# Kernel optimization log

Measured on AMD Instinct MI355X. Metric: run time of the kernel, lower is better.

## Reference

```python
import jax, jax.numpy as jnp
import numpy as np

D_MODEL = 1024
N_HEADS_Q = 16
N_HEADS_KV = 4
D_HEAD = 64  # d_qk = d_v
THETA = 10000.0
CLAMP = 80.0


def apply_rope(x, theta=THETA):
    # x: (b, h, s, d) with d even; interleaved-pair rotary embedding
    b, h, s, d = x.shape
    inv_freq = 1.0 / (theta ** (jnp.arange(0, d, 2, dtype=jnp.float32) / d))  # (d/2,)
    ang = jnp.arange(s, dtype=jnp.float32)[:, None] * inv_freq[None, :]       # (s, d/2)
    cos, sin = jnp.cos(ang), jnp.sin(ang)
    x1, x2 = x[..., 0::2], x[..., 1::2]
    o1 = x1 * cos - x2 * sin
    o2 = x1 * sin + x2 * cos
    return jnp.stack([o1, o2], axis=-1).reshape(b, h, s, d).astype(x.dtype)


def setup_inputs() -> dict:
    key = jax.random.key(0)
    k0, k1, k2, k3, k4 = jax.random.split(key, 5)
    scale = 1.0 / np.sqrt(D_MODEL)
    return {
        "x": jax.random.normal(k0, (2, 2048, D_MODEL), dtype=jnp.float32),
        "Wq": jax.random.normal(k1, (N_HEADS_Q * D_HEAD, D_MODEL), dtype=jnp.float32) * scale,
        "Wk": jax.random.normal(k2, (N_HEADS_KV * D_HEAD, D_MODEL), dtype=jnp.float32) * scale,
        "Wv": jax.random.normal(k3, (N_HEADS_KV * D_HEAD, D_MODEL), dtype=jnp.float32) * scale,
        "Wo": jax.random.normal(k4, (D_MODEL, N_HEADS_Q * D_HEAD), dtype=jnp.float32) * scale,
    }


def _attention(x, Wq, Wk, Wv, Wo):
    b, s, _ = x.shape
    r = N_HEADS_Q // N_HEADS_KV  # queries per KV group
    # projections (Linear: y = x @ W^T, no bias)
    Q = (x @ Wq.T).reshape(b, s, N_HEADS_Q, D_HEAD).transpose(0, 2, 1, 3)   # (b, Hq, s, d)
    K = (x @ Wk.T).reshape(b, s, N_HEADS_KV, D_HEAD).transpose(0, 2, 1, 3)  # (b, Hkv, s, d)
    V = (x @ Wv.T).reshape(b, s, N_HEADS_KV, D_HEAD).transpose(0, 2, 1, 3)
    Q = apply_rope(Q)
    K = apply_rope(K)
    # GQA grouping: (b, Hkv, r, s, d)
    Qg = Q.reshape(b, N_HEADS_KV, r, s, D_HEAD)
    scores = jnp.einsum('bgrqd,bgkd->bgrqk', Qg, K)          # (b, g, r, s, s)
    scores = jnp.clip(scores, -CLAMP, CLAMP)
    causal = jnp.tril(jnp.ones((s, s), dtype=bool))
    scores = jnp.where(causal, scores, -jnp.inf)
    weights = jax.nn.softmax(scores / jnp.sqrt(jnp.float32(D_HEAD)), axis=-1)
    attn = jnp.einsum('bgrqk,bgkd->bgrqd', weights, V)       # (b, g, r, s, d)
    # '... h_kv r s d -> ... s (h_kv r d)'
    attn = attn.transpose(0, 3, 1, 2, 4).reshape(b, s, N_HEADS_Q * D_HEAD)
    return attn @ Wo.T


def reference(x, Wq, Wk, Wv, Wo):
    return _attention(x, Wq, Wk, Wv, Wo)
```

## Files before the change

kernel.cpp:

```cpp
#include <hip/hip_runtime.h>
#include <hip/hip_bf16.h>
#include <math.h>

typedef __attribute__((ext_vector_type(8))) short bf16x8;
typedef __attribute__((ext_vector_type(4))) float f32x4;

#define B_   2
#define S_   2048
#define DM   1024
#define HQ   16
#define HKV  4
#define DH   64

#define MFMA16(a, b, c) __builtin_amdgcn_mfma_f32_16x16x32_bf16(a, b, c, 0, 0, 0)

__device__ __forceinline__ void load_lds16(const __hip_bfloat16* g, __hip_bfloat16* l)
{
    __builtin_amdgcn_global_load_lds(
        (const __attribute__((address_space(1))) unsigned int*)g,
        (__attribute__((address_space(3))) unsigned int*)l, 16, 0, 0);
}

#define CVT_TOTAL 6815744
__global__ void cvt_all(const float* __restrict__ x,  const float* __restrict__ wq,
                        const float* __restrict__ wk, const float* __restrict__ wv,
                        const float* __restrict__ wo,
                        __hip_bfloat16* __restrict__ xb,  __hip_bfloat16* __restrict__ wqb,
                        __hip_bfloat16* __restrict__ wkb, __hip_bfloat16* __restrict__ wvb,
                        __hip_bfloat16* __restrict__ wob)
{
    int i = (blockIdx.x * blockDim.x + threadIdx.x) * 4;
    if (i >= CVT_TOTAL) return;
    const float* src; __hip_bfloat16* dst; int off;
    if      (i < 4194304) { src = x;  dst = xb;  off = 0; }
    else if (i < 5242880) { src = wq; dst = wqb; off = 4194304; }
    else if (i < 5505024) { src = wk; dst = wkb; off = 5242880; }
    else if (i < 5767168) { src = wv; dst = wvb; off = 5505024; }
    else                  { src = wo; dst = wob; off = 5767168; }
    i -= off;
    float4 v = *(const float4*)(src + i);
    union { ushort4 u; __hip_bfloat16 h[4]; } p;
    p.h[0] = __float2bfloat16(v.x);
    p.h[1] = __float2bfloat16(v.y);
    p.h[2] = __float2bfloat16(v.z);
    p.h[3] = __float2bfloat16(v.w);
    *(ushort4*)(dst + i) = p.u;
}

template <bool QKV>
__global__ __launch_bounds__(256, 3) void gemm_tile(
    const __hip_bfloat16* __restrict__ A,
    const __hip_bfloat16* __restrict__ W,
    float* __restrict__ C0, __hip_bfloat16* __restrict__ Qb,
    __hip_bfloat16* __restrict__ Kb, __hip_bfloat16* __restrict__ Vt, int K)
{
    const int wave = threadIdx.x >> 6;
    const int lane = threadIdx.x & 63;
    const int quad = lane >> 4;
    const int l16  = lane & 15;
    const int wm = wave >> 1, wn = wave & 1;
    const int m0 = blockIdx.x * 64;
    const int n0 = blockIdx.y * 128;

    __shared__ __align__(16) __hip_bfloat16 As[64 * 32];
    __shared__ __align__(16) __hip_bfloat16 Bs[128 * 32];

    f32x4 acc[2][4] = {};

    for (int k0 = 0; k0 < K; k0 += 32) {
        #pragma unroll
        for (int r = 0; r < 3; ++r) {
            const int m = wave * 3 + r;
            if (m < 4) {
                const int g = m * 64 + lane;
                const int row = g >> 2;
                const int cbs = ((g & 3) - row) & 3;
                load_lds16(A + (size_t)(m0 + row) * K + k0 + cbs * 8, &As[m * 512]);
            } else {
                const int g = (m - 4) * 64 + lane;
                const int row = g >> 2;
                const int cbs = ((g & 3) - row) & 3;
                load_lds16(W + (size_t)(n0 + row) * K + k0 + cbs * 8, &Bs[(m - 4) * 512]);
            }
        }
        __syncthreads();
        bf16x8 af[2], bf[4];
        #pragma unroll
        for (int i = 0; i < 2; ++i) {
            const int ra = wm * 32 + i * 16 + l16;
            af[i] = *(const bf16x8*)&As[ra * 32 + ((quad + ra) & 3) * 8];
        }
        #pragma unroll
        for (int j = 0; j < 4; ++j) {
            const int rb = wn * 64 + j * 16 + l16;
            bf[j] = *(const bf16x8*)&Bs[rb * 32 + ((quad + rb) & 3) * 8];
        }
        #pragma unroll
        for (int i = 0; i < 2; ++i)
            #pragma unroll
            for (int j = 0; j < 4; ++j)
                acc[i][j] = MFMA16(af[i], bf[j], acc[i][j]);
        __syncthreads();
    }

    #pragma unroll
    for (int j = 0; j < 4; ++j) {
        const int cbase = n0 + wn * 64 + j * 16;
        const int cb = cbase + l16;
        if (QKV && cbase < 1280) {
            const int ii = (cb >> 1) & 31;
            const float f = exp2f((float)ii * -0.41524101186092f);
            const float f_rev = f * 0.15915494309189535f;
            const bool odd = cb & 1;
            #pragma unroll
            for (int i = 0; i < 2; ++i) {
                #pragma unroll
                for (int reg = 0; reg < 4; ++reg) {
                    const int row = m0 + wm * 32 + i * 16 + quad * 4 + reg;
                    const float v = acc[i][j][reg];
                    const float p = __shfl_xor(v, 1);
                    float rev = (float)(row & (S_ - 1)) * f_rev;
                    rev -= floorf(rev);
                    const float sn = __builtin_amdgcn_sinf(rev);
                    const float cs = __builtin_amdgcn_cosf(rev);
                    const float o = odd ? (p * sn + v * cs) : (v * cs - p * sn);
                    if (cbase < 1024)
                        Qb[(size_t)row * 1024 + cb] = __float2bfloat16(o);
                    else
                        Kb[(size_t)row * 256 + cb - 1024] = __float2bfloat16(o);
                }
            }
        } else {
            #pragma unroll
            for (int i = 0; i < 2; ++i) {
                #pragma unroll
                for (int reg = 0; reg < 4; ++reg) {
                    const int row = m0 + wm * 32 + i * 16 + quad * 4 + reg;
                    const float v = acc[i][j][reg];
                    if (QKV)
                        Vt[((size_t)(row >> 11) * 256 + (cb - 1280)) * S_ +
                           (row & (S_ - 1))] = __float2bfloat16(v);
                    else
                        C0[(size_t)row * 1024 + cb] = v;
                }
            }
        }
    }
}

template <bool MASKED>
__device__ __forceinline__ void softmax_store(
    const f32x4* sacc, int q, int k0, int quad, int l16,
    float& lsum, __hip_bfloat16* PsTile)
{
    #pragma unroll
    for (int nt = 0; nt < 4; ++nt) {
        union { ushort4 u; __hip_bfloat16 h[4]; } pk;
        #pragma unroll
        for (int reg = 0; reg < 4; ++reg) {
            const float sc = fminf(fmaxf(sacc[nt][reg], -80.0f), 80.0f);
            float p = exp2f(fmaf(sc, 0.18033688011112042f,
                                 -14.426950408889634f));
            if (MASKED) {
                const int key = k0 + nt * 16 + quad * 4 + reg;
                p = (key <= q) ? p : 0.0f;
            }
            lsum += p;
            pk.h[reg] = __float2bfloat16(p);
        }
        *(ushort4*)&PsTile[l16 * 72 + nt * 16 + quad * 4] = pk.u;
    }
}

__global__ __launch_bounds__(256, 2) void attn_mfma(
    const __hip_bfloat16* __restrict__ Q,
    const __hip_bfloat16* __restrict__ K,
    const __hip_bfloat16* __restrict__ Vt,
    __hip_bfloat16* __restrict__ ctx)
{
    const int t    = blockIdx.x & 15;
    const int hq   = (blockIdx.x >> 4) & (HQ - 1);
    const int b    = blockIdx.x >> 8;
    const int hkv  = hq >> 2;
    const int wave = threadIdx.x >> 6;
    const int lane = threadIdx.x & 63;
    const int quad = lane >> 4;
    const int l16  = lane & 15;

    const int qlo = t * 64 + wave * 16 + l16;
    const int qhi = (31 - t) * 64 + wave * 16 + l16;

    __shared__ __align__(16) __hip_bfloat16 Ks[2][64 * 64];
    __shared__ __align__(16) __hip_bfloat16 Vs[2][64 * 64];
    __shared__ __align__(16) __hip_bfloat16 Ps[4][2][16 * 72];

    const __hip_bfloat16* qpl = Q + ((size_t)(b * S_) + qlo) * (HQ * DH) + hq * DH + quad * 8;
    const __hip_bfloat16* qph = Q + ((size_t)(b * S_) + qhi) * (HQ * DH) + hq * DH + quad * 8;
    bf16x8 ql0 = *(const bf16x8*)qpl;
    bf16x8 ql1 = *(const bf16x8*)(qpl + 32);
    bf16x8 qh0 = *(const bf16x8*)qph;
    bf16x8 qh1 = *(const bf16x8*)(qph + 32);

    const __hip_bfloat16* Kg = K + (size_t)(b * S_) * (HKV * DH) + hkv * DH;
    const __hip_bfloat16* Vg = Vt + (size_t)(b * HKV + hkv) * DH * S_;

    auto stage = [&](int sb, int k0s) {
        #pragma unroll
        for (int r = 0; r < 2; ++r) {
            const int m = wave * 2 + r;
            const int g = m * 64 + lane;
            const int row = g >> 3;
            const int cbs = ((g & 7) - row) & 7;
            load_lds16(Kg + (size_t)(k0s + row) * (HKV * DH) + cbs * 8, &Ks[sb][m * 512]);
            load_lds16(Vg + (size_t)row * S_ + k0s + cbs * 8, &Vs[sb][m * 512]);
        }
    };

    stage(0, 0);

    float lsum_lo = 0.0f, lsum_hi = 0.0f;
    f32x4 Olo[4] = {}, Ohi[4] = {};
    const f32x4 zro = {0.0f, 0.0f, 0.0f, 0.0f};

    const int last = 31 - t;
    for (int kt = 0; kt <= last; ++kt) {
        const int buf = kt & 1;
        const int k0 = kt * 64;
        __syncthreads();
        if (kt < last) stage(buf ^ 1, k0 + 64);
        const bool dual = (kt <= t);

        bf16x8 ka[4][2];
        #pragma unroll
        for (int nt = 0; nt < 4; ++nt) {
            const int key = nt * 16 + l16;
            ka[nt][0] = *(const bf16x8*)&Ks[buf][key * 64 + ((quad + key) & 7) * 8];
            ka[nt][1] = *(const bf16x8*)&Ks[buf][key * 64 + ((quad + 4 + key) & 7) * 8];
        }
        f32x4 shi[4], slo[4];
        #pragma unroll
        for (int nt = 0; nt < 4; ++nt) {
            shi[nt] = MFMA16(ka[nt][0], qh0, zro);
            shi[nt] = MFMA16(ka[nt][1], qh1, shi[nt]);
        }
        if (dual) {
            #pragma unroll
            for (int nt = 0; nt < 4; ++nt) {
                slo[nt] = MFMA16(ka[nt][0], ql0, zro);
                slo[nt] = MFMA16(ka[nt][1], ql1, slo[nt]);
            }
        }

        if (kt == last) softmax_store<true >(shi, qhi, k0, quad, l16, lsum_hi, &Ps[wave][1][0]);
        else            softmax_store<false>(shi, qhi, k0, quad, l16, lsum_hi, &Ps[wave][1][0]);
        if (dual) {
            if (kt == t) softmax_store<true >(slo, qlo, k0, quad, l16, lsum_lo, &Ps[wave][0][0]);
            else         softmax_store<false>(slo, qlo, k0, quad, l16, lsum_lo, &Ps[wave][0][0]);
        }
        __asm__ __volatile__("s_waitcnt lgkmcnt(0)" ::: "memory");

        bf16x8 va[2][4];
        #pragma unroll
        for (int ks = 0; ks < 2; ++ks)
            #pragma unroll
            for (int dt = 0; dt < 4; ++dt) {
                const int d = dt * 16 + l16;
                va[ks][dt] = *(const bf16x8*)
                    &Vs[buf][d * 64 + ((ks * 4 + quad + d) & 7) * 8];
            }
        #pragma unroll
        for (int ks = 0; ks < 2; ++ks) {
            bf16x8 pb = *(const bf16x8*)&Ps[wave][1][l16 * 72 + ks * 32 + quad * 8];
            #pragma unroll
            for (int dt = 0; dt < 4; ++dt)
                Ohi[dt] = MFMA16(va[ks][dt], pb, Ohi[dt]);
        }
        if (dual) {
            #pragma unroll
            for (int ks = 0; ks < 2; ++ks) {
                bf16x8 pb = *(const bf16x8*)&Ps[wave][0][l16 * 72 + ks * 32 + quad * 8];
                #pragma unroll
                for (int dt = 0; dt < 4; ++dt)
                    Olo[dt] = MFMA16(va[ks][dt], pb, Olo[dt]);
            }
        }
    }

    auto finish = [&](float lsum, const f32x4* O, int qrow) {
        lsum += __shfl_xor(lsum, 16);
        lsum += __shfl_xor(lsum, 32);
        const float inv = 1.0f / lsum;
        __hip_bfloat16* cp =
            ctx + ((size_t)(b * S_) + qrow) * (HQ * DH) + hq * DH + quad * 4;
        #pragma unroll
        for (int dt = 0; dt < 4; ++dt) {
            union { ushort4 u; __hip_bfloat16 h[4]; } o;
            #pragma unroll
            for (int reg = 0; reg < 4; ++reg)
                o.h[reg] = __float2bfloat16(O[dt][reg] * inv);
            *(ushort4*)(cp + dt * 16) = o.u;
        }
    };
    finish(lsum_lo, Olo, qlo);
    finish(lsum_hi, Ohi, qhi);
}

extern "C" void kernel_launch(void* const* d_in, const int* in_sizes, int n_in,
                              void* d_out, int out_size, void* d_ws, size_t ws_size,
                              hipStream_t stream)
{
    const float* x  = (const float*)d_in[0];
    const float* Wq = (const float*)d_in[1];
    const float* Wk = (const float*)d_in[2];
    const float* Wv = (const float*)d_in[3];
    const float* Wo = (const float*)d_in[4];
    float* out = (float*)d_out;

    const int M = B_ * S_;

    char* w = (char*)d_ws;
    __hip_bfloat16* xb    = (__hip_bfloat16*)w;  w += (size_t)M * DM * 2;
    __hip_bfloat16* Wqkvb = (__hip_bfloat16*)w;  w += (size_t)1536 * DM * 2;
    __hip_bfloat16* Wob   = (__hip_bfloat16*)w;  w += (size_t)DM * (HQ * DH) * 2;
    __hip_bfloat16* Qb16  = (__hip_bfloat16*)w;  w += (size_t)M * (HQ * DH) * 2;
    __hip_bfloat16* Kb16  = (__hip_bfloat16*)w;  w += (size_t)M * (HKV * DH) * 2;
    __hip_bfloat16* Vt    = (__hip_bfloat16*)w;  w += (size_t)M * (HKV * DH) * 2;
    __hip_bfloat16* ctx   = (__hip_bfloat16*)w;

    __hip_bfloat16* Wqb = Wqkvb;
    __hip_bfloat16* Wkb = Wqkvb + (size_t)1024 * 1024;
    __hip_bfloat16* Wvb = Wqkvb + (size_t)1280 * 1024;

    cvt_all<<<(CVT_TOTAL / 4 + 255) / 256, 256, 0, stream>>>(
        x, Wq, Wk, Wv, Wo, xb, Wqb, Wkb, Wvb, Wob);

    gemm_tile<true><<<dim3(M / 64, 1536 / 128), 256, 0, stream>>>(
        xb, Wqkvb, nullptr, Qb16, Kb16, Vt, DM);

    attn_mfma<<<B_ * HQ * 16, 256, 0, stream>>>(Qb16, Kb16, Vt, ctx);

    gemm_tile<false><<<dim3(M / 64, 1024 / 128), 256, 0, stream>>>(
        ctx, Wob, out, nullptr, nullptr, nullptr, HQ * DH);
}
```

Baseline: 174.0 us.

## Enlarge GEMM tiles to 128x128x64 with double-buffered LDS staging

Rewrites the projection GEMM kernel to use 128x128 output tiles with a K-step of 64, so each wave computes a 4x4 grid of MFMA tiles. Global-to-LDS loads go into a double buffer, so the next K-slice is fetched while the current one is computed, and the barrier count per K-step drops. Per-tile data reuse improves, but block counts are halved (256 and 384 blocks) and LDS/register use rise, which lowers occupancy (launch bounds become 2).

```diff
diff --git a/kernel.cpp b/kernel.cpp
--- a/kernel.cpp
+++ b/kernel.cpp
@@ -48,7 +48,7 @@
 }
 
 template <bool QKV>
-__global__ __launch_bounds__(256, 3) void gemm_tile(
+__global__ __launch_bounds__(256, 2) void gemm_tile(
     const __hip_bfloat16* __restrict__ A,
     const __hip_bfloat16* __restrict__ W,
     float* __restrict__ C0, __hip_bfloat16* __restrict__ Qb,
@@ -59,47 +59,58 @@
     const int quad = lane >> 4;
     const int l16  = lane & 15;
     const int wm = wave >> 1, wn = wave & 1;
-    const int m0 = blockIdx.x * 64;
+    const int m0 = blockIdx.x * 128;
     const int n0 = blockIdx.y * 128;
 
-    __shared__ __align__(16) __hip_bfloat16 As[64 * 32];
-    __shared__ __align__(16) __hip_bfloat16 Bs[128 * 32];
-
-    f32x4 acc[2][4] = {};
-
-    for (int k0 = 0; k0 < K; k0 += 32) {
-        #pragma unroll
-        for (int r = 0; r < 3; ++r) {
-            const int m = wave * 3 + r;
-            if (m < 4) {
-                const int g = m * 64 + lane;
-                const int row = g >> 2;
-                const int cbs = ((g & 3) - row) & 3;
-                load_lds16(A + (size_t)(m0 + row) * K + k0 + cbs * 8, &As[m * 512]);
-            } else {
-                const int g = (m - 4) * 64 + lane;
-                const int row = g >> 2;
-                const int cbs = ((g & 3) - row) & 3;
-                load_lds16(W + (size_t)(n0 + row) * K + k0 + cbs * 8, &Bs[(m - 4) * 512]);
-            }
-        }
-        __syncthreads();
-        bf16x8 af[2], bf[4];
-        #pragma unroll
-        for (int i = 0; i < 2; ++i) {
-            const int ra = wm * 32 + i * 16 + l16;
-            af[i] = *(const bf16x8*)&As[ra * 32 + ((quad + ra) & 3) * 8];
-        }
-        #pragma unroll
-        for (int j = 0; j < 4; ++j) {
-            const int rb = wn * 64 + j * 16 + l16;
-            bf[j] = *(const bf16x8*)&Bs[rb * 32 + ((quad + rb) & 3) * 8];
-        }
-        #pragma unroll
-        for (int i = 0; i < 2; ++i)
-            #pragma unroll
-            for (int j = 0; j < 4; ++j)
-                acc[i][j] = MFMA16(af[i], bf[j], acc[i][j]);
+    __shared__ __align__(16) __hip_bfloat16 As[2][128 * 64];
+    __shared__ __align__(16) __hip_bfloat16 Bs[2][128 * 64];
+
+    f32x4 acc[4][4] = {};
+
+    auto stage = [&](int sb, int kk) {
+        #pragma unroll
+        for (int r = 0; r < 8; ++r) {
+            const int m = wave * 8 + r;
+            const int g = ((m & 15) << 6) | lane;
+            const int row = g >> 3;
+            const int cbs = ((g & 7) - row) & 7;
+            if (m < 16)
+                load_lds16(A + (size_t)(m0 + row) * K + kk + cbs * 8,
+                           &As[sb][(m & 15) * 512]);
+            else
+                load_lds16(W + (size_t)(n0 + row) * K + kk + cbs * 8,
+                           &Bs[sb][(m & 15) * 512]);
+        }
+    };
+
+    const int NT = K >> 6;
+    stage(0, 0);
+    __syncthreads();
+
+    for (int t = 0; t < NT; ++t) {
+        const int buf = t & 1;
+        if (t + 1 < NT) stage(buf ^ 1, (t + 1) << 6);
+        #pragma unroll
+        for (int ks = 0; ks < 2; ++ks) {
+            bf16x8 af[4], bf[4];
+            #pragma unroll
+            for (int i = 0; i < 4; ++i) {
+                const int ra = wm * 64 + i * 16 + l16;
+                af[i] = *(const bf16x8*)
+                    &As[buf][ra * 64 + ((ks * 4 + quad + ra) & 7) * 8];
+            }
+            #pragma unroll
+            for (int j = 0; j < 4; ++j) {
+                const int rb = wn * 64 + j * 16 + l16;
+                bf[j] = *(const bf16x8*)
+                    &Bs[buf][rb * 64 + ((ks * 4 + quad + rb) & 7) * 8];
+            }
+            #pragma unroll
+            for (int i = 0; i < 4; ++i)
+                #pragma unroll
+                for (int j = 0; j < 4; ++j)
+                    acc[i][j] = MFMA16(af[i], bf[j], acc[i][j]);
+        }
         __syncthreads();
     }
 
@@ -113,10 +124,10 @@
             const float f_rev = f * 0.15915494309189535f;
             const bool odd = cb & 1;
             #pragma unroll
-            for (int i = 0; i < 2; ++i) {
+            for (int i = 0; i < 4; ++i) {
                 #pragma unroll
                 for (int reg = 0; reg < 4; ++reg) {
-                    const int row = m0 + wm * 32 + i * 16 + quad * 4 + reg;
+                    const int row = m0 + wm * 64 + i * 16 + quad * 4 + reg;
                     const float v = acc[i][j][reg];
                     const float p = __shfl_xor(v, 1);
                     float rev = (float)(row & (S_ - 1)) * f_rev;
@@ -132,10 +143,10 @@
             }
         } else {
             #pragma unroll
-            for (int i = 0; i < 2; ++i) {
+            for (int i = 0; i < 4; ++i) {
                 #pragma unroll
                 for (int reg = 0; reg < 4; ++reg) {
-                    const int row = m0 + wm * 32 + i * 16 + quad * 4 + reg;
+                    const int row = m0 + wm * 64 + i * 16 + quad * 4 + reg;
                     const float v = acc[i][j][reg];
                     if (QKV)
                         Vt[((size_t)(row >> 11) * 256 + (cb - 1280)) * S_ +
@@ -334,11 +345,11 @@
     cvt_all<<<(CVT_TOTAL / 4 + 255) / 256, 256, 0, stream>>>(
         x, Wq, Wk, Wv, Wo, xb, Wqb, Wkb, Wvb, Wob);
 
-    gemm_tile<true><<<dim3(M / 64, 1536 / 128), 256, 0, stream>>>(
+    gemm_tile<true><<<dim3(M / 128, 1536 / 128), 256, 0, stream>>>(
         xb, Wqkvb, nullptr, Qb16, Kb16, Vt, DM);
 
     attn_mfma<<<B_ * HQ * 16, 256, 0, stream>>>(Qb16, Kb16, Vt, ctx);
 
-    gemm_tile<false><<<dim3(M / 64, 1024 / 128), 256, 0, stream>>>(
+    gemm_tile<false><<<dim3(M / 128, 1024 / 128), 256, 0, stream>>>(
         ctx, Wob, out, nullptr, nullptr, nullptr, HQ * DH);
 }
```

Measured after the change: 165.4 us. 4.9% less time.

## Double-buffer GEMM LDS tiles with BK=64 and raise MFMA priority in attention

Applied to the files above, without the earlier changes.

The projection GEMM now uses a K-tile of 64 instead of 32 and double-buffered LDS, issuing the async global-to-LDS loads for the next tile while computing on the current one. This hides load latency and halves the number of barrier iterations. In the attention loop, s_setprio brackets the MFMA sections so waves doing matrix math get issue priority over waves doing softmax. LDS per block grows to 48KB, which may reduce occupancy under the 3-blocks launch bound. There is also only one barrier per iteration, relying on its placement to prevent the async load overwriting a buffer still being read.

```diff
diff --git a/kernel.cpp b/kernel.cpp
--- a/kernel.cpp
+++ b/kernel.cpp
@@ -62,44 +62,59 @@
     const int m0 = blockIdx.x * 64;
     const int n0 = blockIdx.y * 128;
 
-    __shared__ __align__(16) __hip_bfloat16 As[64 * 32];
-    __shared__ __align__(16) __hip_bfloat16 Bs[128 * 32];
+    __shared__ __align__(16) __hip_bfloat16 As[2][64 * 64];
+    __shared__ __align__(16) __hip_bfloat16 Bs[2][128 * 64];
 
     f32x4 acc[2][4] = {};
 
-    for (int k0 = 0; k0 < K; k0 += 32) {
-        #pragma unroll
-        for (int r = 0; r < 3; ++r) {
-            const int m = wave * 3 + r;
-            if (m < 4) {
-                const int g = m * 64 + lane;
-                const int row = g >> 2;
-                const int cbs = ((g & 3) - row) & 3;
-                load_lds16(A + (size_t)(m0 + row) * K + k0 + cbs * 8, &As[m * 512]);
+    auto stage = [&](int sb, int kk) {
+        #pragma unroll
+        for (int r = 0; r < 6; ++r) {
+            const int m = wave * 6 + r;
+            if (m < 8) {
+                const int g = (m << 6) | lane;
+                const int row = g >> 3;
+                const int cbs = ((g & 7) - row) & 7;
+                load_lds16(A + (size_t)(m0 + row) * K + kk + cbs * 8,
+                           &As[sb][m * 512]);
             } else {
-                const int g = (m - 4) * 64 + lane;
-                const int row = g >> 2;
-                const int cbs = ((g & 3) - row) & 3;
-                load_lds16(W + (size_t)(n0 + row) * K + k0 + cbs * 8, &Bs[(m - 4) * 512]);
-            }
-        }
-        __syncthreads();
-        bf16x8 af[2], bf[4];
-        #pragma unroll
-        for (int i = 0; i < 2; ++i) {
-            const int ra = wm * 32 + i * 16 + l16;
-            af[i] = *(const bf16x8*)&As[ra * 32 + ((quad + ra) & 3) * 8];
-        }
-        #pragma unroll
-        for (int j = 0; j < 4; ++j) {
-            const int rb = wn * 64 + j * 16 + l16;
-            bf[j] = *(const bf16x8*)&Bs[rb * 32 + ((quad + rb) & 3) * 8];
-        }
-        #pragma unroll
-        for (int i = 0; i < 2; ++i)
-            #pragma unroll
-            for (int j = 0; j < 4; ++j)
-                acc[i][j] = MFMA16(af[i], bf[j], acc[i][j]);
+                const int g = ((m - 8) << 6) | lane;
+                const int row = g >> 3;
+                const int cbs = ((g & 7) - row) & 7;
+                load_lds16(W + (size_t)(n0 + row) * K + kk + cbs * 8,
+                           &Bs[sb][(m - 8) * 512]);
+            }
+        }
+    };
+
+    const int NT = K >> 6;
+    stage(0, 0);
+    __syncthreads();
+
+    for (int t = 0; t < NT; ++t) {
+        const int buf = t & 1;
+        if (t + 1 < NT) stage(buf ^ 1, (t + 1) << 6);
+        #pragma unroll
+        for (int ks = 0; ks < 2; ++ks) {
+            bf16x8 af[2], bf[4];
+            #pragma unroll
+            for (int i = 0; i < 2; ++i) {
+                const int ra = wm * 32 + i * 16 + l16;
+                af[i] = *(const bf16x8*)
+                    &As[buf][ra * 64 + ((ks * 4 + quad + ra) & 7) * 8];
+            }
+            #pragma unroll
+            for (int j = 0; j < 4; ++j) {
+                const int rb = wn * 64 + j * 16 + l16;
+                bf[j] = *(const bf16x8*)
+                    &Bs[buf][rb * 64 + ((ks * 4 + quad + rb) & 7) * 8];
+            }
+            #pragma unroll
+            for (int i = 0; i < 2; ++i)
+                #pragma unroll
+                for (int j = 0; j < 4; ++j)
+                    acc[i][j] = MFMA16(af[i], bf[j], acc[i][j]);
+        }
         __syncthreads();
     }
 
@@ -238,6 +253,7 @@
             ka[nt][1] = *(const bf16x8*)&Ks[buf][key * 64 + ((quad + 4 + key) & 7) * 8];
         }
         f32x4 shi[4], slo[4];
+        __builtin_amdgcn_s_setprio(1);
         #pragma unroll
         for (int nt = 0; nt < 4; ++nt) {
             shi[nt] = MFMA16(ka[nt][0], qh0, zro);
@@ -250,6 +266,7 @@
                 slo[nt] = MFMA16(ka[nt][1], ql1, slo[nt]);
             }
         }
+        __builtin_amdgcn_s_setprio(0);
 
         if (kt == last) softmax_store<true >(shi, qhi, k0, quad, l16, lsum_hi, &Ps[wave][1][0]);
         else            softmax_store<false>(shi, qhi, k0, quad, l16, lsum_hi, &Ps[wave][1][0]);
@@ -268,6 +285,7 @@
                 va[ks][dt] = *(const bf16x8*)
                     &Vs[buf][d * 64 + ((ks * 4 + quad + d) & 7) * 8];
             }
+        __builtin_amdgcn_s_setprio(1);
         #pragma unroll
         for (int ks = 0; ks < 2; ++ks) {
             bf16x8 pb = *(const bf16x8*)&Ps[wave][1][l16 * 72 + ks * 32 + quad * 8];
@@ -284,6 +302,7 @@
                     Olo[dt] = MFMA16(va[ks][dt], pb, Olo[dt]);
             }
         }
+        __builtin_amdgcn_s_setprio(0);
     }
 
     auto finish = [&](float lsum, const f32x4* O, int qrow) {
```

Result: faster. 168.0 us (-3.5%).
